# Performance work log

Hardware: AMD Instinct MI355X
Metric: run time of the kernel (lower is better)

## Reference

```python
import math
import jax, jax.numpy as jnp
import numpy as np

N, MA, DESIGN, RADIAL, SOFTENING, RM = 8, 24, 26, 15, 3, 5.0


def setup_inputs() -> dict:
    key = jax.random.key(0)
    k1, k2 = jax.random.split(key, 2)
    # atomic coordinates, spread out so interatomic distances are realistic (bohr)
    coords = jax.random.normal(k1, (N, MA, 3), jnp.float32) * 3.0
    # labels all >= 0 -> full padding (padding[i] == MA for every molecule)
    labels = jax.random.randint(k2, (N, MA), 0, 10)
    # deterministic synthetic Lebedev-like design (26 points on the unit sphere)
    phi = jnp.linspace(0.0, 2.0 * math.pi, DESIGN, endpoint=False).astype(jnp.float32)
    psi = jnp.linspace(0.1, math.pi - 0.1, DESIGN).astype(jnp.float32)
    sphere = jnp.stack([jnp.cos(phi) * jnp.sin(psi),
                        jnp.sin(phi) * jnp.sin(psi),
                        jnp.cos(psi)], axis=1)           # [D, 3]
    sphere_weights = jnp.full((DESIGN,), 1.0 / DESIGN, dtype=jnp.float32)
    return {"labels": labels, "coords": coords,
            "sphere": sphere, "sphere_weights": sphere_weights}


def _spheric_grid(sphere, sphere_weights):
    # Gauss-Chebyshev radial quadrature mapped by the Becke transform
    i = jnp.arange(1, RADIAL + 1, dtype=jnp.float32)
    z = -jnp.cos(math.pi * (2.0 * i - 1.0) / (2.0 * RADIAL))
    dr = 2.0 * RM * (1.0 - z) ** -2
    r = RM * (1.0 + z) / (1.0 - z)
    w = jnp.sqrt(1.0 - z ** 2) * dr * math.pi / RADIAL
    w = r ** 2 * 4.0 * math.pi * w                       # [R]
    conc = (r[:, None, None] * sphere[None]).reshape(-1, 3)          # [R*D, 3]
    wt = (sphere_weights[None, :] * w[:, None]).reshape(-1)          # [R*D]
    return conc, wt


def _becke(x, r, dm, idx):
    # x [n, mx, 3] grid points, r [n, M, 3] centers, dm [n, M, M], idx [mx]
    rx = jnp.linalg.norm(x[:, :, None, :] - r[:, None, :, :], axis=-1)   # [n, mx, M]
    # elliptic coordinate mu_ij for every grid point: [n, mx, M, M]
    mu = (rx[..., :, None] - rx[..., None, :]) / jnp.clip(dm[:, None], 1e-12, None)
    for _ in range(1, SOFTENING):                       # softening passes
        mu = 0.5 * mu * (3.0 - mu ** 2)
    mu = 0.5 * (1.0 - mu)
    mu = mu + 0.5 * jnp.eye(dm.shape[-1], dtype=x.dtype)  # diagonal -> 1
    cell = jnp.prod(mu, axis=-1)                        # [n, mx, M] cell functions
    v_i = jnp.take_along_axis(cell, idx[None, :, None], axis=2)[..., 0]
    return v_i / cell.sum(axis=2)


def reference(labels, coords, sphere, sphere_weights):
    # labels are all >= 0 here, so padding == MA for every molecule and the
    # original per-molecule loop collapses into one batched computation.
    conc, wt = _spheric_grid(sphere, sphere_weights)    # conc [ms,3], wt [ms]
    ms = conc.shape[0]
    n, M, _ = coords.shape
    dm = jnp.linalg.norm(coords[:, :, None, :] - coords[:, None, :, :], axis=-1)
    # place concentric spheres on each atom (atom-major ordering, as in torch)
    grid = (coords[:, :, None, :] + conc[None, None]).reshape(n, M * ms, 3)
    w_full = jnp.broadcast_to(wt[None, :], (M, ms)).reshape(-1)      # [M*ms]
    idx = jnp.repeat(jnp.arange(M), ms)                              # sample -> center
    v = _becke(grid, coords, dm, idx)                                # [n, M*ms]
    weights = v * w_full[None, :]
    dv = grid[:, :, None, :] - coords[:, None, :, :]                 # [n, M*ms, M, 3]
    return grid, dv, weights
```

## Files before the change

kernel.cpp:

```cpp
#include <hip/hip_runtime.h>
#include <math.h>

constexpr int MAC = 24;
constexpr int DES = 26;
constexpr int RAD = 15;
constexpr int MS  = RAD * DES;
constexpr int MX  = MAC * MS;
constexpr int PPG = 6;
constexpr int NPR = PPG / 2;
constexpr int GPB = 8;
constexpr int PPB = PPG * GPB;
constexpr int BPM = MX / PPB;

typedef float v2f __attribute__((ext_vector_type(2)));

__device__ __forceinline__ v2f pk_add(v2f a, v2f b) {
    v2f d; asm("v_pk_add_f32 %0, %1, %2" : "=v"(d) : "v"(a), "v"(b)); return d;
}
__device__ __forceinline__ v2f pk_mul(v2f a, v2f b) {
    v2f d; asm("v_pk_mul_f32 %0, %1, %2" : "=v"(d) : "v"(a), "v"(b)); return d;
}
__device__ __forceinline__ v2f pk_fma(v2f a, v2f b, v2f c) {
    v2f d; asm("v_pk_fma_f32 %0, %1, %2, %3" : "=v"(d) : "v"(a), "v"(b), "v"(c)); return d;
}

template <int M>
__device__ __forceinline__ float xorswz(float v) {
    return __int_as_float(__builtin_amdgcn_ds_swizzle(__float_as_int(v), (M << 10) | 0x1f));
}

__global__ __launch_bounds__(256) void becke_pre(
    const float* __restrict__ coords, const float* __restrict__ sphere,
    const float* __restrict__ sw, int nmol,
    float* __restrict__ inv_dm, float4* __restrict__ conc4, float4* __restrict__ cpad)
{
    const int e = blockIdx.x * 256 + threadIdx.x;
    const int nidm = nmol * MAC * MAC;
    if (e < nidm) {
        int n = e / (MAC * MAC), r0 = e - n * MAC * MAC;
        int i = r0 / MAC, j = r0 - i * MAC;
        const float* cb = coords + n * MAC * 3;
        float dx = cb[i * 3 + 0] - cb[j * 3 + 0];
        float dy = cb[i * 3 + 1] - cb[j * 3 + 1];
        float dz = cb[i * 3 + 2] - cb[j * 3 + 2];
        float dd = sqrtf(dx * dx + dy * dy + dz * dz);
        inv_dm[e] = 1.0f / fmaxf(dd, 1e-12f);
        return;
    }
    const int e2 = e - nidm;
    if (e2 < MS) {
        int k = e2 / DES, d = e2 - k * DES;
        double i   = (double)k + 1.0;
        double z   = -cos(M_PI * (2.0 * i - 1.0) / (2.0 * (double)RAD));
        double omz = 1.0 - z;
        double dr  = 10.0 / (omz * omz);
        double r   = 5.0 * (1.0 + z) / omz;
        double w1  = sqrt(1.0 - z * z) * dr * M_PI / (double)RAD;
        double w   = r * r * 4.0 * M_PI * w1;
        conc4[e2] = make_float4((float)(r * (double)sphere[d * 3 + 0]),
                                (float)(r * (double)sphere[d * 3 + 1]),
                                (float)(r * (double)sphere[d * 3 + 2]),
                                (float)((double)sw[d] * w));
        return;
    }
    const int e3 = e2 - MS;
    if (e3 < nmol * MAC) {
        cpad[e3] = make_float4(coords[e3 * 3 + 0], coords[e3 * 3 + 1],
                               coords[e3 * 3 + 2], 0.0f);
    }
}

__global__ __launch_bounds__(256) void becke_main(
    const float4* __restrict__ cpad,
    const float*  __restrict__ inv_dm,
    const float4* __restrict__ conc4,
    float* __restrict__ og,
    float* __restrict__ odv,
    float* __restrict__ ow)
{
    __shared__ v2f rxp[GPB][NPR][32];

    const int tid = threadIdx.x;
    const int l   = tid & 31;
    const int grp = tid >> 5;
    const int b   = blockIdx.x;
    const int n   = b / BPM;
    const int bm  = b - n * BPM;
    const int s0  = bm * PPB + grp * PPG;
    const bool act = (l < MAC);
    const int  i   = act ? l : (MAC - 1);

    const float4 ci = cpad[n * MAC + i];

    int ap[PPG];
    float gx[PPG], gy[PPG], gz[PPG], wt[PPG], rx[PPG];
    const size_t sgb = (size_t)n * MX + s0;
    float* dvp = odv + (sgb * MAC + i) * 3;

    #pragma unroll
    for (int p = 0; p < PPG; ++p) {
        int sp = s0 + p;
        ap[p] = sp / MS;
        int tp = sp - ap[p] * MS;
        float4 cc = conc4[tp];
        float4 ca = cpad[n * MAC + ap[p]];
        gx[p] = ca.x + cc.x;
        gy[p] = ca.y + cc.y;
        gz[p] = ca.z + cc.z;
        wt[p] = cc.w;
        float dx = gx[p] - ci.x;
        float dy = gy[p] - ci.y;
        float dz = gz[p] - ci.z;
        if (act) {
            dvp[p * MAC * 3 + 0] = dx;
            dvp[p * MAC * 3 + 1] = dy;
            dvp[p * MAC * 3 + 2] = dz;
        }
        rx[p] = __builtin_amdgcn_sqrtf(dx * dx + dy * dy + dz * dz);
    }
    #pragma unroll
    for (int q = 0; q < NPR; ++q)
        rxp[grp][q][l] = (v2f){-rx[2 * q], -rx[2 * q + 1]};
    __builtin_amdgcn_wave_barrier();

    float inv[MAC];
    {
        const float* irow = inv_dm + (n * MAC + i) * MAC;
        #pragma unroll
        for (int q = 0; q < MAC / 4; ++q) {
            float4 v = *reinterpret_cast<const float4*>(irow + q * 4);
            inv[q * 4 + 0] = v.x; inv[q * 4 + 1] = v.y;
            inv[q * 4 + 2] = v.z; inv[q * 4 + 3] = v.w;
        }
    }

    const v2f cm05 = {-0.5f, -0.5f}, c15 = {1.5f, 1.5f}, c05 = {0.5f, 0.5f};
    v2f prodq[NPR] = {{1.0f, 1.0f}, {1.0f, 1.0f}, {1.0f, 1.0f}};
    v2f rxi2[NPR];
    #pragma unroll
    for (int q = 0; q < NPR; ++q) rxi2[q] = (v2f){rx[2 * q], rx[2 * q + 1]};

    #pragma unroll
    for (int jj = 0; jj < MAC / 2; ++jj) {
        const v2f iva = {inv[2 * jj],     inv[2 * jj]};
        const v2f ivb = {inv[2 * jj + 1], inv[2 * jj + 1]};
        #pragma unroll
        for (int q = 0; q < NPR; ++q) {
            float4 v4 = *reinterpret_cast<const float4*>(&rxp[grp][q][2 * jj]);
            v2f mu = pk_mul(pk_add(rxi2[q], (v2f){v4.x, v4.y}), iva);
            mu = pk_mul(mu, pk_fma(pk_mul(mu, mu), cm05, c15));
            mu = pk_mul(mu, pk_fma(pk_mul(mu, mu), cm05, c15));
            prodq[q] = pk_mul(prodq[q], pk_fma(mu, cm05, c05));
            v2f mv = pk_mul(pk_add(rxi2[q], (v2f){v4.z, v4.w}), ivb);
            mv = pk_mul(mv, pk_fma(pk_mul(mv, mv), cm05, c15));
            mv = pk_mul(mv, pk_fma(pk_mul(mv, mv), cm05, c15));
            prodq[q] = pk_mul(prodq[q], pk_fma(mv, cm05, c05));
        }
    }

    const v2f am = act ? (v2f){2.0f, 2.0f} : (v2f){0.0f, 0.0f};
    v2f cellq[NPR];
    #pragma unroll
    for (int q = 0; q < NPR; ++q) cellq[q] = pk_mul(prodq[q], am);

    #pragma unroll
    for (int p = 0; p < PPG; ++p) {
        float c  = (p & 1) ? cellq[p >> 1].y : cellq[p >> 1].x;
        float su = c;
        su += xorswz<1>(su);
        su += xorswz<2>(su);
        su += xorswz<4>(su);
        su += xorswz<8>(su);
        su += xorswz<16>(su);
        if (l == ap[p])
            ow[sgb + p] = c * __builtin_amdgcn_rcpf(su) * wt[p];
    }

    if (l >= MAC && l < MAC + PPG) {
        int p = l - MAC;
        float* gp = og + (sgb + p) * 3;
        gp[0] = gx[p]; gp[1] = gy[p]; gp[2] = gz[p];
    }
}

extern "C" void kernel_launch(void* const* d_in, const int* in_sizes, int n_in,
                              void* d_out, int out_size, void* d_ws, size_t ws_size,
                              hipStream_t stream) {
    const float* coords = (const float*)d_in[1];
    const float* sphere = (const float*)d_in[2];
    const float* sw     = (const float*)d_in[3];

    const int nmol = in_sizes[1] / (MAC * 3);

    float*  ws     = (float*)d_ws;
    float*  inv_dm = ws;
    float4* conc4  = (float4*)(inv_dm + (size_t)nmol * MAC * MAC);
    float4* cpad   = conc4 + MS;

    float* o     = (float*)d_out;
    float* ogrid = o;
    float* odv   = ogrid + (size_t)nmol * MX * 3;
    float* owt   = odv + (size_t)nmol * MX * MAC * 3;

    const int pre_elems  = nmol * MAC * MAC + MS + nmol * MAC;
    const int pre_blocks = (pre_elems + 255) / 256;
    becke_pre<<<dim3(pre_blocks), dim3(256), 0, stream>>>(
        coords, sphere, sw, nmol, inv_dm, conc4, cpad);

    becke_main<<<dim3(nmol * BPM), dim3(256), 0, stream>>>(
        cpad, inv_dm, conc4, ogrid, odv, owt);
}
```

Measured before the change: 83.41 us.

## Cut points per wave to two, use DPP reductions and compiler packed math

Each wave now handles two grid points instead of six, which triples the block count and shrinks per-thread register state. An occupancy hint is added to the launch bounds. The inline-asm packed add and multiply become plain vector arithmetic, and the pack FMA becomes an elementwise builtin, so the compiler can schedule them. The first four cross-lane reduction steps move from ds_swizzle to DPP (quad perm, then half-row and row mirror), with a swizzle kept only for the last step. The risk is that each lane now reloads the inverse distance row and coordinates for fewer points, which adds redundant loads and setup work per point.

Result: faster. 79.55 us (-4.6%).

```diff
diff --git a/kernel.cpp b/kernel.cpp
--- a/kernel.cpp
+++ b/kernel.cpp
@@ -6,27 +6,25 @@
 constexpr int RAD = 15;
 constexpr int MS  = RAD * DES;
 constexpr int MX  = MAC * MS;
-constexpr int PPG = 6;
-constexpr int NPR = PPG / 2;
+constexpr int PPG = 2;
 constexpr int GPB = 8;
 constexpr int PPB = PPG * GPB;
 constexpr int BPM = MX / PPB;
 
 typedef float v2f __attribute__((ext_vector_type(2)));
 
-__device__ __forceinline__ v2f pk_add(v2f a, v2f b) {
-    v2f d; asm("v_pk_add_f32 %0, %1, %2" : "=v"(d) : "v"(a), "v"(b)); return d;
-}
-__device__ __forceinline__ v2f pk_mul(v2f a, v2f b) {
-    v2f d; asm("v_pk_mul_f32 %0, %1, %2" : "=v"(d) : "v"(a), "v"(b)); return d;
-}
 __device__ __forceinline__ v2f pk_fma(v2f a, v2f b, v2f c) {
-    v2f d; asm("v_pk_fma_f32 %0, %1, %2, %3" : "=v"(d) : "v"(a), "v"(b), "v"(c)); return d;
+    return __builtin_elementwise_fma(a, b, c);
 }
 
 template <int M>
 __device__ __forceinline__ float xorswz(float v) {
     return __int_as_float(__builtin_amdgcn_ds_swizzle(__float_as_int(v), (M << 10) | 0x1f));
+}
+template <int CTRL>
+__device__ __forceinline__ float dppx(float v) {
+    return __int_as_float(__builtin_amdgcn_update_dpp(
+        0, __float_as_int(v), CTRL, 0xf, 0xf, true));
 }
 
 __global__ __launch_bounds__(256) void becke_pre(
@@ -70,7 +68,7 @@
     }
 }
 
-__global__ __launch_bounds__(256) void becke_main(
+__global__ __launch_bounds__(256, 4) void becke_main(
     const float4* __restrict__ cpad,
     const float*  __restrict__ inv_dm,
     const float4* __restrict__ conc4,
@@ -78,7 +76,7 @@
     float* __restrict__ odv,
     float* __restrict__ ow)
 {
-    __shared__ v2f rxp[GPB][NPR][32];
+    __shared__ v2f rxp[GPB][32];
 
     const int tid = threadIdx.x;
     const int l   = tid & 31;
@@ -118,9 +116,7 @@
         }
         rx[p] = __builtin_amdgcn_sqrtf(dx * dx + dy * dy + dz * dz);
     }
-    #pragma unroll
-    for (int q = 0; q < NPR; ++q)
-        rxp[grp][q][l] = (v2f){-rx[2 * q], -rx[2 * q + 1]};
+    rxp[grp][l] = (v2f){rx[0], rx[1]};
     __builtin_amdgcn_wave_barrier();
 
     float inv[MAC];
@@ -135,42 +131,34 @@
     }
 
     const v2f cm05 = {-0.5f, -0.5f}, c15 = {1.5f, 1.5f}, c05 = {0.5f, 0.5f};
-    v2f prodq[NPR] = {{1.0f, 1.0f}, {1.0f, 1.0f}, {1.0f, 1.0f}};
-    v2f rxi2[NPR];
-    #pragma unroll
-    for (int q = 0; q < NPR; ++q) rxi2[q] = (v2f){rx[2 * q], rx[2 * q + 1]};
+    const v2f rxi = {rx[0], rx[1]};
+    v2f prod = {1.0f, 1.0f};
 
     #pragma unroll
     for (int jj = 0; jj < MAC / 2; ++jj) {
+        float4 v4 = *reinterpret_cast<const float4*>(&rxp[grp][2 * jj]);
         const v2f iva = {inv[2 * jj],     inv[2 * jj]};
         const v2f ivb = {inv[2 * jj + 1], inv[2 * jj + 1]};
-        #pragma unroll
-        for (int q = 0; q < NPR; ++q) {
-            float4 v4 = *reinterpret_cast<const float4*>(&rxp[grp][q][2 * jj]);
-            v2f mu = pk_mul(pk_add(rxi2[q], (v2f){v4.x, v4.y}), iva);
-            mu = pk_mul(mu, pk_fma(pk_mul(mu, mu), cm05, c15));
-            mu = pk_mul(mu, pk_fma(pk_mul(mu, mu), cm05, c15));
-            prodq[q] = pk_mul(prodq[q], pk_fma(mu, cm05, c05));
-            v2f mv = pk_mul(pk_add(rxi2[q], (v2f){v4.z, v4.w}), ivb);
-            mv = pk_mul(mv, pk_fma(pk_mul(mv, mv), cm05, c15));
-            mv = pk_mul(mv, pk_fma(pk_mul(mv, mv), cm05, c15));
-            prodq[q] = pk_mul(prodq[q], pk_fma(mv, cm05, c05));
-        }
-    }
-
-    const v2f am = act ? (v2f){2.0f, 2.0f} : (v2f){0.0f, 0.0f};
-    v2f cellq[NPR];
-    #pragma unroll
-    for (int q = 0; q < NPR; ++q) cellq[q] = pk_mul(prodq[q], am);
+        v2f mu = (rxi - (v2f){v4.x, v4.y}) * iva;
+        mu = mu * pk_fma(mu * mu, cm05, c15);
+        mu = mu * pk_fma(mu * mu, cm05, c15);
+        prod = prod * pk_fma(mu, cm05, c05);
+        v2f mv = (rxi - (v2f){v4.z, v4.w}) * ivb;
+        mv = mv * pk_fma(mv * mv, cm05, c15);
+        mv = mv * pk_fma(mv * mv, cm05, c15);
+        prod = prod * pk_fma(mv, cm05, c05);
+    }
+
+    const v2f cell = prod * (act ? (v2f){2.0f, 2.0f} : (v2f){0.0f, 0.0f});
 
     #pragma unroll
     for (int p = 0; p < PPG; ++p) {
-        float c  = (p & 1) ? cellq[p >> 1].y : cellq[p >> 1].x;
+        float c  = (p == 0) ? cell.x : cell.y;
         float su = c;
-        su += xorswz<1>(su);
-        su += xorswz<2>(su);
-        su += xorswz<4>(su);
-        su += xorswz<8>(su);
+        su += dppx<0xB1>(su);
+        su += dppx<0x4E>(su);
+        su += dppx<0x141>(su);
+        su += dppx<0x140>(su);
         su += xorswz<16>(su);
         if (l == ap[p])
             ow[sgb + p] = c * __builtin_amdgcn_rcpf(su) * wt[p];
```
